# Performance work log

Hardware: AMD Instinct MI355X
Metric: run time of the kernel (lower is better)

Reference implementation:

```python
import jax, jax.numpy as jnp
import numpy as np

GATE_DIM = 1313 + 622  # hardcoded in the module
D1 = 300
D2 = 300
OUT = 300


def setup_inputs() -> dict:
    key = jax.random.key(0)
    ks = jax.random.split(key, 12)
    N, M = 384, 384
    inp = {
        "feature1": jax.random.normal(ks[0], (N, GATE_DIM), jnp.float32),
        "box1": jax.random.uniform(ks[1], (N, 5), jnp.float32),
        "feature2": jax.random.normal(ks[2], (M, GATE_DIM), jnp.float32),
        "box2": jax.random.uniform(ks[3], (M, 5), jnp.float32),
        "attrlabel_embeddings": jax.random.normal(ks[4], (GATE_DIM, D1), jnp.float32) * 0.05,
        # learned parameters
        "gate1": 10.0 * jnp.ones((GATE_DIM,), jnp.float32),
        "gate2": 10.0 * jnp.ones((GATE_DIM,), jnp.float32),
        "weight_loc": jnp.zeros((2,), jnp.float32),
        "fc1_w": jax.random.normal(ks[5], (OUT, D1 + D2), jnp.float32) * (1.0 / np.sqrt(D1 + D2)),
        "fc1_b": jnp.zeros((OUT,), jnp.float32),
        "fc2_w": jax.random.normal(ks[6], (OUT, 10), jnp.float32) * (1.0 / np.sqrt(10.0)),
        "fc2_b": jnp.zeros((OUT,), jnp.float32),
        "fc3_w": jax.random.normal(ks[7], (OUT, OUT), jnp.float32) * (1.0 / np.sqrt(OUT)),
        "fc3_b": jnp.zeros((OUT,), jnp.float32),
    }
    return inp


def _preprocess(feature, box):
    # repo's preprocess callable; modeled as identity on the feature
    # (feature already has dim input_dim1/input_dim2 expected by fc1)
    return feature


def reference(feature1, box1, feature2, box2, attrlabel_embeddings,
              gate1, gate2, weight_loc,
              fc1_w, fc1_b, fc2_w, fc2_b, fc3_w, fc3_b):
    # gated feature -> attrlabel embedding projection
    f1 = (feature1 * jax.nn.sigmoid(gate1)) @ attrlabel_embeddings  # [N, D1]
    f1 = _preprocess(f1, box1)
    f2 = (feature2 * jax.nn.sigmoid(gate2)) @ attrlabel_embeddings  # [M, D2]
    f2 = _preprocess(f2, box2)

    # fc1(cat(meshgrid(f1,f2))) == f1@W_a^T (broadcast over M) + f2@W_b^T (broadcast over N) + b
    Wa, Wb = fc1_w[:, :f1.shape[-1]], fc1_w[:, f1.shape[-1]:]
    semantic = jax.nn.relu(
        jnp.einsum('nd,od->no', f1, Wa)[:, None, :]
        + jnp.einsum('md,od->mo', f2, Wb)[None, :, :]
        + fc1_b
    )  # [N, M, OUT]

    Wa2, Wb2 = fc2_w[:, :5], fc2_w[:, 5:]
    spatial = jax.nn.relu(
        jnp.einsum('nd,od->no', box1, Wa2)[:, None, :]
        + jnp.einsum('md,od->mo', box2, Wb2)[None, :, :]
        + fc2_b
    )  # [N, M, OUT]

    w = jax.nn.softmax(weight_loc)
    mixed = w[0] * semantic + w[1] * spatial
    embedding = jnp.einsum('nmo,po->nmp', mixed, fc3_w) + fc3_b  # [N, M, OUT]
    return embedding
```

## Files before the change

### kernel.cpp

```cpp
#include <hip/hip_runtime.h>
#include <hip/hip_bf16.h>

#define NROW 384
#define GD   1935
#define GK   1952
#define DD   300
#define KP   320
#define DP   304

#define OFF_XBF  4112
#define OFF_EBT  753680
#define OFF_FC1B 1066000
#define OFF_FC3B 1168400
#define OFF_F1B  1217040
#define OFF_AB   1339920
#define OFF_CD   1585680

typedef short short8 __attribute__((ext_vector_type(8)));
typedef float floatx4 __attribute__((ext_vector_type(4)));

__device__ inline unsigned short f2bf(float x){
  union { float f; unsigned u; } v; v.f = x;
  unsigned r = v.u + 0x7fffu + ((v.u >> 16) & 1u);
  return (unsigned short)(r >> 16);
}

#define TX  (2*24*61*64)
#define TE  (20*61*64)
#define TF1 (2*320*40)
#define TF3 (190*64)
#define TTOT (TX+TE+TF1+TF3)
__global__ void k_cvt_all(const float* f1, const float* f2, const float* E,
                          const float* g1, const float* g2,
                          const float* fc1w, const float* fc3w, float* ws){
  int t = blockIdx.x * 256 + threadIdx.x;
  unsigned short* xbf = (unsigned short*)(ws + OFF_XBF);
  unsigned short* ebt = (unsigned short*)(ws + OFF_EBT);
  unsigned short* f1b = (unsigned short*)(ws + OFF_FC1B);
  unsigned short* f3b = (unsigned short*)(ws + OFF_FC3B);
  if (t < TX){
    int lane = t & 63;
    int rem  = t >> 6;
    int kc = rem % 61;
    int rem2 = rem / 61;
    int mt = rem2 % 24, z = rem2 / 24;
    const float* X = z ? f2 : f1;
    const float* g = z ? g2 : g1;
    int n  = mt*16 + (lane & 15);
    int k0 = kc*32 + (lane >> 4)*8;
    union { unsigned short s[8]; uint4 v; } u;
    #pragma unroll
    for (int e = 0; e < 8; ++e){
      int k = k0 + e;
      float v = 0.f;
      if (k < GD){
        float sg = 1.f / (1.f + expf(-g[k]));
        v = X[n*GD + k] * sg;
      }
      u.s[e] = f2bf(v);
    }
    *(uint4*)&xbf[(size_t)t * 8] = u.v;
  } else if (t < TX + TE){
    int i = t - TX;
    int lane = i & 63;
    int rem = i >> 6;
    int kc = rem % 61, ct = rem / 61;
    int c  = ct*16 + (lane & 15);
    int k0 = kc*32 + (lane >> 4)*8;
    union { unsigned short s[8]; uint4 v; } u;
    #pragma unroll
    for (int e = 0; e < 8; ++e){
      int k = k0 + e;
      float v = (k < GD && c < DD) ? E[k*DD + c] : 0.f;
      u.s[e] = f2bf(v);
    }
    *(uint4*)&ebt[(size_t)i * 8] = u.v;
  } else if (t < TX + TE + TF1){
    int i = t - TX - TE;
    int d8 = i % 40; int o = (i/40) % 320; int z = i / (40*320);
    int d0 = d8*8;
    union { unsigned short s[8]; uint4 v; } u;
    #pragma unroll
    for (int e = 0; e < 8; ++e){
      int d = d0 + e;
      float v = (o < DD && d < DD) ? fc1w[o*(2*DD) + z*DD + d] : 0.f;
      u.s[e] = f2bf(v);
    }
    *(uint4*)&f1b[(size_t)((z*KP + o)*KP + d0)] = u.v;
  } else if (t < TTOT){
    int i = t - TX - TE - TF1;
    int lane = i & 63; int g = i >> 6;
    int pt = g % 19, kc = g / 19;
    int p  = pt*16 + (lane & 15);
    int k0 = kc*32 + (lane >> 4)*8;
    union { unsigned short s[8]; uint4 v; } u;
    #pragma unroll
    for (int e = 0; e < 8; ++e){
      int k = k0 + e;
      float v = (p < DD && k < DD) ? fc3w[p*DD + k] : 0.f;
      u.s[e] = f2bf(v);
    }
    *(uint4*)&f3b[(size_t)i * 8] = u.v;
  }
}

__global__ __launch_bounds__(256) void k_gg(float* ws){
  int z = blockIdx.y;
  const unsigned short* XP = (const unsigned short*)(ws + OFF_XBF) + (size_t)z*24*61*512;
  const unsigned short* EP = (const unsigned short*)(ws + OFF_EBT);
  unsigned short* out      = (unsigned short*)(ws + OFF_F1B) + z*384*KP;
  int t = threadIdx.x, lane = t & 63;
  int id = blockIdx.x * 4 + (t >> 6);
  int mt = id / 20, ct = id - mt*20;
  int col = lane & 15, quad = lane >> 4;
  const unsigned short* ap = XP + (size_t)mt*61*512 + lane*8;
  const unsigned short* bp = EP + (size_t)ct*61*512 + lane*8;
  floatx4 acc = (floatx4){0.f,0.f,0.f,0.f};
  for (int kc = 0; kc < 61; ++kc){
    short8 a = *(const short8*)(ap + kc*512);
    short8 b = *(const short8*)(bp + kc*512);
    acc = __builtin_amdgcn_mfma_f32_16x16x32_bf16(a, b, acc, 0, 0, 0);
  }
  int c = ct*16 + col;
  #pragma unroll
  for (int r = 0; r < 4; ++r){
    int m = mt*16 + quad*4 + r;
    out[m*KP + c] = (c < DD) ? f2bf(acc[r]) : (unsigned short)0;
  }
}

__global__ __launch_bounds__(256) void k_sesp(const float* fc1b, const float* box1,
                      const float* box2, const float* fc2w, const float* fc2b,
                      const float* wloc, float* ws){
  int z = blockIdx.y;
  float wa = wloc[0], wbv = wloc[1];
  float mm = fmaxf(wa, wbv);
  float ea = expf(wa - mm), eb = expf(wbv - mm);
  float w0 = ea / (ea + eb), w1 = eb / (ea + eb);
  int t = threadIdx.x;
  if (blockIdx.x < 120){
    const unsigned short* F = (const unsigned short*)(ws + OFF_F1B) + z*384*KP;
    const unsigned short* W = (const unsigned short*)(ws + OFF_FC1B) + z*KP*KP;
    int lane = t & 63;
    int id = blockIdx.x * 4 + (t >> 6);
    int rt = id / 20, ot = id - rt*20;
    int col = lane & 15, quad = lane >> 4;
    const unsigned short* ap = F + (rt*16 + col)*KP + quad*8;
    const unsigned short* bp = W + (ot*16 + col)*KP + quad*8;
    floatx4 acc = (floatx4){0.f,0.f,0.f,0.f};
    #pragma unroll
    for (int kc = 0; kc < 10; ++kc){
      short8 a = *(const short8*)(ap + kc*32);
      short8 b = *(const short8*)(bp + kc*32);
      acc = __builtin_amdgcn_mfma_f32_16x16x32_bf16(a, b, acc, 0, 0, 0);
    }
    int o = ot*16 + col;
    if (z == 0){
      float bias = (o < DD) ? fc1b[o] : 0.f;
      float* outp = ws + OFF_AB;
      #pragma unroll
      for (int r = 0; r < 4; ++r){
        int rr = rt*16 + quad*4 + r;
        outp[rr*KP + o] = (o < DD) ? w0 * (acc[r] + bias) : 0.f;
      }
    } else {
      float* BP = ws + OFF_AB + 384*KP;
      int kcs = o >> 5, q_o = (o >> 3) & 3, e = o & 7;
      #pragma unroll
      for (int r = 0; r < 4; ++r){
        int lm = quad*4 + r;
        BP[(rt*10 + kcs)*512 + (q_o*16 + lm)*8 + e] = (o < DD) ? w0 * acc[r] : 0.f;
      }
    }
  } else {
    int tt = (blockIdx.x - 120) * 256 + t;
    int r = tt / KP, o = tt - r*KP;
    const float* bx = z ? box2 : box1;
    int joff = z ? 5 : 0;
    float v = 0.f;
    if (o < DD){
      const float* b = bx + r * 5;
      const float* wr = fc2w + o * 10 + joff;
      v = b[0]*wr[0] + b[1]*wr[1] + b[2]*wr[2] + b[3]*wr[3] + b[4]*wr[4];
      if (!z) v += fc2b[o];
      v *= w1;
    }
    if (z == 0) ws[OFF_CD + tt] = v;
    else {
      float* DPp = ws + OFF_CD + 384*KP;
      int mt = r >> 4, lm = r & 15, kcs = o >> 5, q_o = (o >> 3) & 3, e = o & 7;
      DPp[(mt*10 + kcs)*512 + (q_o*16 + lm)*8 + e] = v;
    }
  }
}

__global__ __launch_bounds__(512, 3) void k_main(const float* fc3b, float* out, const float* ws){
  __shared__ __align__(16) unsigned short wbuf[2][19*512];
  const unsigned short* fc3p = (const unsigned short*)(ws + OFF_FC3B);
  int t = threadIdx.x;
  int lane = t & 63, wave = t >> 6;
  int col = lane & 15, quad = lane >> 4;
  int n = blockIdx.y;
  int mt = blockIdx.x * 8 + wave;
  const float* Ah = ws + OFF_AB + n * KP;
  const float* Ch = ws + OFF_CD + n * KP;
  const float* BP = ws + OFF_AB + 384*KP + (size_t)mt*10*512 + lane*8;
  const float* DPp = ws + OFF_CD + 384*KP + (size_t)mt*10*512 + lane*8;

  floatx4 acc[19];
  #pragma unroll
  for (int i = 0; i < 19; ++i) acc[i] = (floatx4){0.f,0.f,0.f,0.f};

  {
    const uint4* src = (const uint4*)fc3p;
    uint4* dst = (uint4*)&wbuf[0][0];
    dst[t] = src[t];
    dst[t + 512] = src[t + 512];
    if (t < 192) dst[t + 1024] = src[t + 1024];
  }
  __syncthreads();

  for (int kc = 0; kc < 10; ++kc){
    uint4 s0, s1, s2;
    bool pre = (kc < 9);
    if (pre){
      const uint4* src = (const uint4*)(fc3p + (size_t)(kc+1) * (19*512));
      s0 = src[t]; s1 = src[t + 512];
      if (t < 192) s2 = src[t + 1024];
    }
    int kb = kc*32 + quad*8;
    union { unsigned short s[8]; short8 v8; } u;
    float4 a0 = *(const float4*)(Ah + kb);
    float4 c0 = *(const float4*)(Ch + kb);
    float4 b0 = *(const float4*)(BP + kc*512);
    float4 d0 = *(const float4*)(DPp + kc*512);
    float4 a1 = *(const float4*)(Ah + kb + 4);
    float4 c1 = *(const float4*)(Ch + kb + 4);
    float4 b1 = *(const float4*)(BP + kc*512 + 4);
    float4 d1 = *(const float4*)(DPp + kc*512 + 4);
    u.s[0] = f2bf(fmaxf(a0.x + b0.x, 0.f) + fmaxf(c0.x + d0.x, 0.f));
    u.s[1] = f2bf(fmaxf(a0.y + b0.y, 0.f) + fmaxf(c0.y + d0.y, 0.f));
    u.s[2] = f2bf(fmaxf(a0.z + b0.z, 0.f) + fmaxf(c0.z + d0.z, 0.f));
    u.s[3] = f2bf(fmaxf(a0.w + b0.w, 0.f) + fmaxf(c0.w + d0.w, 0.f));
    u.s[4] = f2bf(fmaxf(a1.x + b1.x, 0.f) + fmaxf(c1.x + d1.x, 0.f));
    u.s[5] = f2bf(fmaxf(a1.y + b1.y, 0.f) + fmaxf(c1.y + d1.y, 0.f));
    u.s[6] = f2bf(fmaxf(a1.z + b1.z, 0.f) + fmaxf(c1.z + d1.z, 0.f));
    u.s[7] = f2bf(fmaxf(a1.w + b1.w, 0.f) + fmaxf(c1.w + d1.w, 0.f));
    short8 af = u.v8;
    const unsigned short* wb = wbuf[kc & 1];
    #pragma unroll
    for (int pt = 0; pt < 19; ++pt){
      short8 bf = *(const short8*)(wb + pt*512 + lane*8);
      acc[pt] = __builtin_amdgcn_mfma_f32_16x16x32_bf16(af, bf, acc[pt], 0, 0, 0);
    }
    if (pre){
      uint4* dst = (uint4*)&wbuf[(kc + 1) & 1][0];
      dst[t] = s0; dst[t + 512] = s1;
      if (t < 192) dst[t + 1024] = s2;
    }
    __syncthreads();
  }

  #pragma unroll
  for (int pt = 0; pt < 19; ++pt){
    int p = pt*16 + col;
    if (p < DD){
      float bias = fc3b[p];
      #pragma unroll
      for (int r = 0; r < 4; ++r){
        int m = mt*16 + quad*4 + r;
        out[((size_t)n * NROW + m) * DD + p] = acc[pt][r] + bias;
      }
    }
  }
}

extern "C" void kernel_launch(void* const* d_in, const int* in_sizes, int n_in,
                              void* d_out, int out_size, void* d_ws, size_t ws_size,
                              hipStream_t stream) {
  const float* feature1 = (const float*)d_in[0];
  const float* box1     = (const float*)d_in[1];
  const float* feature2 = (const float*)d_in[2];
  const float* box2     = (const float*)d_in[3];
  const float* E        = (const float*)d_in[4];
  const float* gate1    = (const float*)d_in[5];
  const float* gate2    = (const float*)d_in[6];
  const float* wloc     = (const float*)d_in[7];
  const float* fc1w     = (const float*)d_in[8];
  const float* fc1b     = (const float*)d_in[9];
  const float* fc2w     = (const float*)d_in[10];
  const float* fc2b     = (const float*)d_in[11];
  const float* fc3w     = (const float*)d_in[12];
  const float* fc3b     = (const float*)d_in[13];
  float* out = (float*)d_out;
  float* ws  = (float*)d_ws;

  hipLaunchKernelGGL(k_cvt_all, dim3((TTOT + 255)/256), dim3(256), 0, stream,
                     feature1, feature2, E, gate1, gate2, fc1w, fc3w, ws);
  hipLaunchKernelGGL(k_gg, dim3(120, 2), dim3(256), 0, stream, ws);
  hipLaunchKernelGGL(k_sesp, dim3(600, 2), dim3(256), 0, stream,
                     fc1b, box1, box2, fc2w, fc2b, wloc, ws);
  hipLaunchKernelGGL(k_main, dim3(3, NROW), dim3(512), 0, stream, fc3b, out, ws);
}
```

Measured before the change: 331.9 us.

## Retile main GEMM to 6-wave blocks, prefetch activation operands, and use nontemporal stores

The main fused relu-mix plus fc3 GEMM kernel now uses 384-thread blocks (6 waves), each covering 6 m-tiles, on a 4x384 grid instead of 512 threads on 3x384. The per-k-chunk A/B/C/D fp32 operand loads are register double-buffered one iteration ahead. The end-of-loop __syncthreads is replaced by an explicit lgkmcnt wait plus raw s_barrier, and it is skipped on the last iteration. Output writes use nontemporal stores. The aim is to hide global-load latency, reduce barrier overhead, change the occupancy balance and avoid polluting cache with the large output, at the cost of more live registers.

```diff
diff --git a/kernel.cpp b/kernel.cpp
--- a/kernel.cpp
+++ b/kernel.cpp
@@ -194,17 +194,17 @@
   }
 }
 
-__global__ __launch_bounds__(512, 3) void k_main(const float* fc3b, float* out, const float* ws){
+__global__ __launch_bounds__(384, 3) void k_main(const float* fc3b, float* out, const float* ws){
   __shared__ __align__(16) unsigned short wbuf[2][19*512];
   const unsigned short* fc3p = (const unsigned short*)(ws + OFF_FC3B);
   int t = threadIdx.x;
   int lane = t & 63, wave = t >> 6;
   int col = lane & 15, quad = lane >> 4;
   int n = blockIdx.y;
-  int mt = blockIdx.x * 8 + wave;
+  int mt = blockIdx.x * 6 + wave;
   const float* Ah = ws + OFF_AB + n * KP;
   const float* Ch = ws + OFF_CD + n * KP;
-  const float* BP = ws + OFF_AB + 384*KP + (size_t)mt*10*512 + lane*8;
+  const float* BP  = ws + OFF_AB + 384*KP + (size_t)mt*10*512 + lane*8;
   const float* DPp = ws + OFF_CD + 384*KP + (size_t)mt*10*512 + lane*8;
 
   floatx4 acc[19];
@@ -214,30 +214,36 @@
   {
     const uint4* src = (const uint4*)fc3p;
     uint4* dst = (uint4*)&wbuf[0][0];
-    dst[t] = src[t];
-    dst[t + 512] = src[t + 512];
-    if (t < 192) dst[t + 1024] = src[t + 1024];
-  }
+    dst[t] = src[t]; dst[t + 384] = src[t + 384]; dst[t + 768] = src[t + 768];
+    if (t < 64) dst[t + 1152] = src[t + 1152];
+  }
+  float4 na0 = *(const float4*)(Ah + quad*8);
+  float4 na1 = *(const float4*)(Ah + quad*8 + 4);
+  float4 nc0 = *(const float4*)(Ch + quad*8);
+  float4 nc1 = *(const float4*)(Ch + quad*8 + 4);
+  float4 nb0 = *(const float4*)(BP);
+  float4 nb1 = *(const float4*)(BP + 4);
+  float4 nd0 = *(const float4*)(DPp);
+  float4 nd1 = *(const float4*)(DPp + 4);
   __syncthreads();
 
   for (int kc = 0; kc < 10; ++kc){
-    uint4 s0, s1, s2;
     bool pre = (kc < 9);
+    uint4 s0, s1, s2, s3;
     if (pre){
       const uint4* src = (const uint4*)(fc3p + (size_t)(kc+1) * (19*512));
-      s0 = src[t]; s1 = src[t + 512];
-      if (t < 192) s2 = src[t + 1024];
-    }
-    int kb = kc*32 + quad*8;
+      s0 = src[t]; s1 = src[t + 384]; s2 = src[t + 768];
+      if (t < 64) s3 = src[t + 1152];
+    }
+    float4 a0=na0, a1=na1, b0=nb0, b1=nb1, c0=nc0, c1=nc1, d0=nd0, d1=nd1;
+    if (pre){
+      int kb = (kc+1)*32 + quad*8;
+      na0 = *(const float4*)(Ah + kb);   na1 = *(const float4*)(Ah + kb + 4);
+      nc0 = *(const float4*)(Ch + kb);   nc1 = *(const float4*)(Ch + kb + 4);
+      nb0 = *(const float4*)(BP + (kc+1)*512);  nb1 = *(const float4*)(BP + (kc+1)*512 + 4);
+      nd0 = *(const float4*)(DPp + (kc+1)*512); nd1 = *(const float4*)(DPp + (kc+1)*512 + 4);
+    }
     union { unsigned short s[8]; short8 v8; } u;
-    float4 a0 = *(const float4*)(Ah + kb);
-    float4 c0 = *(const float4*)(Ch + kb);
-    float4 b0 = *(const float4*)(BP + kc*512);
-    float4 d0 = *(const float4*)(DPp + kc*512);
-    float4 a1 = *(const float4*)(Ah + kb + 4);
-    float4 c1 = *(const float4*)(Ch + kb + 4);
-    float4 b1 = *(const float4*)(BP + kc*512 + 4);
-    float4 d1 = *(const float4*)(DPp + kc*512 + 4);
     u.s[0] = f2bf(fmaxf(a0.x + b0.x, 0.f) + fmaxf(c0.x + d0.x, 0.f));
     u.s[1] = f2bf(fmaxf(a0.y + b0.y, 0.f) + fmaxf(c0.y + d0.y, 0.f));
     u.s[2] = f2bf(fmaxf(a0.z + b0.z, 0.f) + fmaxf(c0.z + d0.z, 0.f));
@@ -255,10 +261,12 @@
     }
     if (pre){
       uint4* dst = (uint4*)&wbuf[(kc + 1) & 1][0];
-      dst[t] = s0; dst[t + 512] = s1;
-      if (t < 192) dst[t + 1024] = s2;
-    }
-    __syncthreads();
+      dst[t] = s0; dst[t + 384] = s1; dst[t + 768] = s2;
+      if (t < 64) dst[t + 1152] = s3;
+      asm volatile("s_waitcnt lgkmcnt(0)" ::: "memory");
+      __builtin_amdgcn_s_barrier();
+      __builtin_amdgcn_sched_barrier(0);
+    }
   }
 
   #pragma unroll
@@ -269,7 +277,8 @@
       #pragma unroll
       for (int r = 0; r < 4; ++r){
         int m = mt*16 + quad*4 + r;
-        out[((size_t)n * NROW + m) * DD + p] = acc[pt][r] + bias;
+        __builtin_nontemporal_store(acc[pt][r] + bias,
+                                    &out[((size_t)n * NROW + m) * DD + p]);
       }
     }
   }
@@ -300,5 +309,5 @@
   hipLaunchKernelGGL(k_gg, dim3(120, 2), dim3(256), 0, stream, ws);
   hipLaunchKernelGGL(k_sesp, dim3(600, 2), dim3(256), 0, stream,
                      fc1b, box1, box2, fc2w, fc2b, wloc, ws);
-  hipLaunchKernelGGL(k_main, dim3(3, NROW), dim3(512), 0, stream, fc3b, out, ws);
-}
+  hipLaunchKernelGGL(k_main, dim3(4, NROW), dim3(384), 0, stream, fc3b, out, ws);
+}
```

Measured after the change: 370.4 us. 1.12x slower.
